# Performance work log

Measured on AMD Instinct MI355X. Metric: run time of the kernel, lower is better.

Reference implementation:

```python
import jax, jax.numpy as jnp
import numpy as np

B = 2048        # graphs
MAX_LEN = 254   # nodes per graph (pad target)
DIM = 64
NF = 78         # num_features_xd
DEG = 8
N = B * MAX_LEN         # 520192 nodes
E = N * DEG             # 4161536 edges
BN_EPS = 1e-5
LN_EPS = 1e-5


def setup_inputs() -> dict:
    key = jax.random.key(0)
    ks = jax.random.split(key, 24)
    x = jax.random.normal(ks[0], (N, NF), jnp.float32)
    # intra-graph random edges: (src, dst) within the same graph
    g = jax.random.randint(ks[1], (E,), 0, B)
    src = g * MAX_LEN + jax.random.randint(ks[2], (E,), 0, MAX_LEN)
    dst = g * MAX_LEN + jax.random.randint(ks[3], (E,), 0, MAX_LEN)
    edge_index = jnp.stack([src, dst]).astype(jnp.int32)
    batch = (jnp.arange(N) // MAX_LEN).astype(jnp.int32)
    batch_len = jnp.full((B,), MAX_LEN, jnp.int32)

    def lin(k, fan_in, shape):
        return jax.random.uniform(k, shape, jnp.float32, -1.0, 1.0) / np.sqrt(fan_in)

    # conv1 MLP: 78->64->64
    w1a = lin(ks[4], NF, (NF, DIM)); b1a = lin(ks[5], NF, (DIM,))
    w1b = lin(ks[6], DIM, (DIM, DIM)); b1b = lin(ks[7], DIM, (DIM,))
    # convs 2-5 stacked: 64->64->64
    Wa = lin(ks[8], DIM, (4, DIM, DIM)); ba = lin(ks[9], DIM, (4, DIM))
    Wb = lin(ks[10], DIM, (4, DIM, DIM)); bb = lin(ks[11], DIM, (4, DIM))
    bn_gamma = jnp.ones((5, DIM), jnp.float32)
    bn_beta = jnp.zeros((5, DIM), jnp.float32)
    fc_w = lin(ks[12], DIM, (DIM, DIM)); fc_b = lin(ks[13], DIM, (DIM,))
    ln_gamma = jnp.ones((DIM,), jnp.float32)
    ln_beta = jnp.zeros((DIM,), jnp.float32)
    return {
        "x": x, "edge_index": edge_index, "batch": batch,
        "batch_len": batch_len, "max_len": MAX_LEN,
        "w1a": w1a, "b1a": b1a, "w1b": w1b, "b1b": b1b,
        "Wa": Wa, "ba": ba, "Wb": Wb, "bb": bb,
        "bn_gamma": bn_gamma, "bn_beta": bn_beta,
        "fc_w": fc_w, "fc_b": fc_b,
        "ln_gamma": ln_gamma, "ln_beta": ln_beta,
    }


def _gin_layer(h, src, dst, n, W1, b1, W2, b2, gamma, beta):
    # GINConv (eps=0): z_i = MLP(x_i + sum_{j->i} x_j), then ReLU, then BatchNorm (batch stats)
    agg = jax.ops.segment_sum(h[src], dst, num_segments=n)
    z = h + agg
    z = jnp.maximum(z @ W1 + b1, 0.0) @ W2 + b2
    z = jnp.maximum(z, 0.0)
    mean = z.mean(axis=0)
    var = jnp.square(z - mean).mean(axis=0)  # biased var, as torch BN training
    return (z - mean) * jax.lax.rsqrt(var + BN_EPS) * gamma + beta


def reference(x, edge_index, batch, batch_len, max_len,
              w1a, b1a, w1b, b1b, Wa, ba, Wb, bb,
              bn_gamma, bn_beta, fc_w, fc_b, ln_gamma, ln_beta):
    n = x.shape[0]
    src, dst = edge_index[0], edge_index[1]
    h = _gin_layer(x, src, dst, n, w1a, b1a, w1b, b1b, bn_gamma[0], bn_beta[0])
    for i in range(4):
        h = _gin_layer(h, src, dst, n, Wa[i], ba[i], Wb[i], bb[i],
                       bn_gamma[i + 1], bn_beta[i + 1])
    # get_nodes_att_f: pad per-graph node features to [B, max_len, dim]
    nb = batch_len.shape[0]
    offsets = jnp.cumsum(batch_len) - batch_len            # start index of each graph
    pos = jnp.arange(n, dtype=jnp.int32) - offsets[batch]  # node position within graph
    x_seq = jnp.zeros((nb, max_len, h.shape[1]), h.dtype).at[batch, pos].set(h)
    # global_add_pool + fc + relu + (dropout eval: identity) + layernorm
    pooled = jax.ops.segment_sum(h, batch, num_segments=nb)
    y = jnp.maximum(pooled @ fc_w + fc_b, 0.0)
    mu = y.mean(axis=-1, keepdims=True)
    var = jnp.square(y - mu).mean(axis=-1, keepdims=True)
    y = (y - mu) * jax.lax.rsqrt(var + LN_EPS) * ln_gamma + ln_beta
    return (x_seq, y)
```

## Files before the change

kernel.cpp:

```cpp
#include <hip/hip_runtime.h>

#define NGRAPH 2048
#define MAXLEN 254
#define NNODE 520192
#define NEDGE 4161536
#define NF 78
#define CAP 32
#define BN_EPS 1e-5f
#define LN_EPS 1e-5f

__global__ __launch_bounds__(256) void k_init(int* __restrict__ deg, float* __restrict__ stats) {
    int i = blockIdx.x * 256 + threadIdx.x;
    deg[i] = 0;
    if (blockIdx.x == 0) {
        for (int j = threadIdx.x; j < 5 * 128; j += 256) stats[j] = 0.f;
    }
}

__global__ __launch_bounds__(256) void k_build(const int* __restrict__ ei,
                                               int* __restrict__ deg,
                                               unsigned char* __restrict__ elist) {
    int e = blockIdx.x * 256 + threadIdx.x;
    int s = ei[e];
    int d = ei[NEDGE + e];
    int g = d / MAXLEN;
    int r = atomicAdd(&deg[d], 1);
    elist[(size_t)d * CAP + r] = (unsigned char)(s - g * MAXLEN);
}

template <int FOLD>
__global__ __launch_bounds__(256) void k_gather(const float* __restrict__ h,
                                                const unsigned char* __restrict__ elist,
                                                const int* __restrict__ deg,
                                                const float* __restrict__ stats,
                                                const float* __restrict__ gamma,
                                                const float* __restrict__ beta,
                                                float* __restrict__ acc) {
    const int CHUNK = (NNODE * 16 / 256) / 8;
    int lb = (int)(blockIdx.x & 7) * CHUNK + (int)(blockIdx.x >> 3);
    size_t t = (size_t)lb * 256 + threadIdx.x;
    int node = (int)(t >> 4);
    int g4 = (int)(t & 15) * 4;
    int dg = deg[node];
    int base = (node / MAXLEN) * MAXLEN;
    const float4 h0 = *(const float4*)(h + ((size_t)node << 6) + g4);
    float a0 = h0.x, a1 = h0.y, a2 = h0.z, a3 = h0.w;
    const unsigned* row = (const unsigned*)(elist + (size_t)node * CAP);
    int ne4 = (dg + 3) >> 2;
    for (int e4 = 0; e4 < ne4; e4++) {
        unsigned pk = row[e4];
#pragma unroll
        for (int j = 0; j < 4; j++) {
            if (4 * e4 + j < dg) {
                int s = base + (int)((pk >> (8 * j)) & 255u);
                float4 v = *(const float4*)(h + ((size_t)s << 6) + g4);
                a0 += v.x; a1 += v.y; a2 += v.z; a3 += v.w;
            }
        }
    }
    if (FOLD) {
        const float invN = 1.0f / NNODE;
        float k = (float)(1 + dg);
        float r[4] = {a0, a1, a2, a3};
#pragma unroll
        for (int j = 0; j < 4; j++) {
            float mean = stats[g4 + j] * invN;
            float var = stats[64 + g4 + j] * invN - mean * mean;
            float sc = gamma[g4 + j] * rsqrtf(var + BN_EPS);
            float bi = beta[g4 + j] - mean * sc;
            r[j] = r[j] * sc + k * bi;
        }
        a0 = r[0]; a1 = r[1]; a2 = r[2]; a3 = r[3];
    }
    *(float4*)(acc + ((size_t)node << 6) + g4) = make_float4(a0, a1, a2, a3);
}

__global__ __launch_bounds__(256) void k_gemm78(const float* __restrict__ x,
                                                const float* __restrict__ W,
                                                float* __restrict__ out) {
    __shared__ float sW[NF * 64];
    for (int i = threadIdx.x; i < NF * 64; i += 256) sW[i] = W[i];
    __syncthreads();
    int node = blockIdx.x * 256 + threadIdx.x;
    const float* xr = x + (size_t)node * NF;
    float a[64];
#pragma unroll
    for (int c = 0; c < 64; c++) a[c] = 0.f;
    for (int k2 = 0; k2 < NF / 2; k2++) {
        float2 xv = ((const float2*)xr)[k2];
        const float* w0 = sW + (2 * k2) * 64;
#pragma unroll
        for (int c = 0; c < 64; c++) a[c] += xv.x * w0[c];
#pragma unroll
        for (int c = 0; c < 64; c++) a[c] += xv.y * w0[64 + c];
    }
    float* orow = out + ((size_t)node << 6);
#pragma unroll
    for (int c = 0; c < 64; c += 4)
        *(float4*)(orow + c) = make_float4(a[c], a[c + 1], a[c + 2], a[c + 3]);
}

__device__ __forceinline__ void second_matmul(const float (&a)[64], const float* __restrict__ sW2,
                                              const float* __restrict__ sb2,
                                              float* __restrict__ orow) {
#pragma unroll
    for (int cb = 0; cb < 64; cb += 16) {
        float o[16];
#pragma unroll
        for (int j = 0; j < 16; j++) o[j] = sb2[cb + j];
#pragma unroll
        for (int k = 0; k < 64; k++) {
            float ak = a[k];
#pragma unroll
            for (int j = 0; j < 16; j++) o[j] += ak * sW2[k * 64 + cb + j];
        }
#pragma unroll
        for (int j = 0; j < 16; j += 4)
            *(float4*)(orow + cb + j) =
                make_float4(fmaxf(o[j], 0.f), fmaxf(o[j + 1], 0.f),
                            fmaxf(o[j + 2], 0.f), fmaxf(o[j + 3], 0.f));
    }
}

__global__ __launch_bounds__(256) void k_mlp_tail(const float* __restrict__ zin,
                                                  const float* __restrict__ b1,
                                                  const float* __restrict__ W2,
                                                  const float* __restrict__ b2,
                                                  float* __restrict__ out) {
    __shared__ float sW2[64 * 64];
    __shared__ float sb1[64], sb2[64];
    for (int i = threadIdx.x; i < 64 * 64; i += 256) sW2[i] = W2[i];
    if (threadIdx.x < 64) { sb1[threadIdx.x] = b1[threadIdx.x]; sb2[threadIdx.x] = b2[threadIdx.x]; }
    __syncthreads();
    int node = blockIdx.x * 256 + threadIdx.x;
    const float* zr = zin + ((size_t)node << 6);
    float a[64];
#pragma unroll
    for (int c = 0; c < 64; c += 4) {
        float4 v = *(const float4*)(zr + c);
        a[c]     = fmaxf(v.x + sb1[c], 0.f);
        a[c + 1] = fmaxf(v.y + sb1[c + 1], 0.f);
        a[c + 2] = fmaxf(v.z + sb1[c + 2], 0.f);
        a[c + 3] = fmaxf(v.w + sb1[c + 3], 0.f);
    }
    second_matmul(a, sW2, sb2, out + ((size_t)node << 6));
}

__global__ __launch_bounds__(256) void k_mlp_dual(const float* __restrict__ zin,
                                                  const float* __restrict__ W1,
                                                  const float* __restrict__ b1,
                                                  const float* __restrict__ W2,
                                                  const float* __restrict__ b2,
                                                  float* __restrict__ out) {
    __shared__ float sW1[64 * 64];
    __shared__ float sW2[64 * 64];
    __shared__ float sb1[64], sb2[64];
    for (int i = threadIdx.x; i < 64 * 64; i += 256) { sW1[i] = W1[i]; sW2[i] = W2[i]; }
    if (threadIdx.x < 64) { sb1[threadIdx.x] = b1[threadIdx.x]; sb2[threadIdx.x] = b2[threadIdx.x]; }
    __syncthreads();
    int node = blockIdx.x * 256 + threadIdx.x;
    const float* zr = zin + ((size_t)node << 6);
    float a[64];
#pragma unroll
    for (int c = 0; c < 64; c++) a[c] = sb1[c];
    for (int k4 = 0; k4 < 16; k4++) {
        float4 xv = ((const float4*)zr)[k4];
        const float* w = sW1 + k4 * 256;
#pragma unroll
        for (int c = 0; c < 64; c++) a[c] += xv.x * w[c];
#pragma unroll
        for (int c = 0; c < 64; c++) a[c] += xv.y * w[64 + c];
#pragma unroll
        for (int c = 0; c < 64; c++) a[c] += xv.z * w[128 + c];
#pragma unroll
        for (int c = 0; c < 64; c++) a[c] += xv.w * w[192 + c];
    }
#pragma unroll
    for (int c = 0; c < 64; c++) a[c] = fmaxf(a[c], 0.f);
    second_matmul(a, sW2, sb2, out + ((size_t)node << 6));
}

__global__ __launch_bounds__(256) void k_bnstats(const float* __restrict__ h,
                                                 float* __restrict__ stats) {
    __shared__ float ss[128];
    if (threadIdx.x < 128) ss[threadIdx.x] = 0.f;
    __syncthreads();
    int tid = blockIdx.x * 256 + threadIdx.x;
    int c4 = (tid & 15) * 4;
    float s0 = 0, s1 = 0, s2 = 0, s3 = 0, q0 = 0, q1 = 0, q2 = 0, q3 = 0;
    const float4* p = (const float4*)h;
    for (size_t i = tid; i < (size_t)NNODE * 16; i += 65536) {
        float4 v = p[i];
        s0 += v.x; q0 += v.x * v.x;
        s1 += v.y; q1 += v.y * v.y;
        s2 += v.z; q2 += v.z * v.z;
        s3 += v.w; q3 += v.w * v.w;
    }
    atomicAdd(&ss[c4], s0);      atomicAdd(&ss[c4 + 1], s1);
    atomicAdd(&ss[c4 + 2], s2);  atomicAdd(&ss[c4 + 3], s3);
    atomicAdd(&ss[64 + c4], q0); atomicAdd(&ss[64 + c4 + 1], q1);
    atomicAdd(&ss[64 + c4 + 2], q2); atomicAdd(&ss[64 + c4 + 3], q3);
    __syncthreads();
    if (threadIdx.x < 128) atomicAdd(&stats[threadIdx.x], ss[threadIdx.x]);
}

__global__ __launch_bounds__(256) void k_bnapply(float* __restrict__ h,
                                                 const float* __restrict__ stats,
                                                 const float* __restrict__ gamma,
                                                 const float* __restrict__ beta) {
    size_t i = (size_t)blockIdx.x * 256 + threadIdx.x;
    int c0 = (int)(i & 15) * 4;
    const float invN = 1.0f / NNODE;
    float4 v = ((const float4*)h)[i];
    float sc[4], bi[4];
#pragma unroll
    for (int j = 0; j < 4; j++) {
        float mean = stats[c0 + j] * invN;
        float var = stats[64 + c0 + j] * invN - mean * mean;
        float s = gamma[c0 + j] * rsqrtf(var + BN_EPS);
        sc[j] = s;
        bi[j] = beta[c0 + j] - mean * s;
    }
    v.x = v.x * sc[0] + bi[0];
    v.y = v.y * sc[1] + bi[1];
    v.z = v.z * sc[2] + bi[2];
    v.w = v.w * sc[3] + bi[3];
    ((float4*)h)[i] = v;
}

__global__ __launch_bounds__(256) void k_final(const float* __restrict__ h,
                                               const float* __restrict__ fcw,
                                               const float* __restrict__ fcb,
                                               const float* __restrict__ lng,
                                               const float* __restrict__ lnb,
                                               float* __restrict__ y) {
    int b = blockIdx.x;
    int q = threadIdx.x >> 6;
    int c = threadIdx.x & 63;
    const float* base = h + (size_t)b * MAXLEN * 64;
    float s = 0.f;
    for (int p = q; p < MAXLEN; p += 4) s += base[p * 64 + c];
    __shared__ float sp[4][64];
    sp[q][c] = s;
    __syncthreads();
    __shared__ float pooled[64];
    if (threadIdx.x < 64) pooled[c] = sp[0][c] + sp[1][c] + sp[2][c] + sp[3][c];
    __syncthreads();
    if (threadIdx.x < 64) {
        float accv = fcb[c];
        for (int k = 0; k < 64; k++) accv += pooled[k] * fcw[k * 64 + c];
        accv = fmaxf(accv, 0.f);
        float t = accv;
        for (int o = 32; o; o >>= 1) t += __shfl_xor(t, o, 64);
        float mu = t * (1.0f / 64.0f);
        float d = accv - mu;
        float t2 = d * d;
        for (int o = 32; o; o >>= 1) t2 += __shfl_xor(t2, o, 64);
        float var = t2 * (1.0f / 64.0f);
        y[(size_t)b * 64 + c] = d * rsqrtf(var + LN_EPS) * lng[c] + lnb[c];
    }
}

extern "C" void kernel_launch(void* const* d_in, const int* in_sizes, int n_in,
                              void* d_out, int out_size, void* d_ws, size_t ws_size,
                              hipStream_t stream) {
    const float* x   = (const float*)d_in[0];
    const int*   ei  = (const int*)d_in[1];
    const float* w1a = (const float*)d_in[5];
    const float* b1a = (const float*)d_in[6];
    const float* w1b = (const float*)d_in[7];
    const float* b1b = (const float*)d_in[8];
    const float* Wa  = (const float*)d_in[9];
    const float* ba  = (const float*)d_in[10];
    const float* Wb  = (const float*)d_in[11];
    const float* bb  = (const float*)d_in[12];
    const float* bng = (const float*)d_in[13];
    const float* bnb = (const float*)d_in[14];
    const float* fcw = (const float*)d_in[15];
    const float* fcb = (const float*)d_in[16];
    const float* lng = (const float*)d_in[17];
    const float* lnb = (const float*)d_in[18];

    float* h   = (float*)d_out;
    float* y   = h + (size_t)NNODE * 64;
    float* acc = (float*)d_ws;
    float* stats = acc + (size_t)NNODE * 64;
    int* deg = (int*)(stats + 5 * 128);
    unsigned char* elist = (unsigned char*)(deg + NNODE);

    const int NB_NODE = NNODE / 256;
    const int NB_VEC  = NNODE * 16 / 256;
    const int NB_EDGE = NEDGE / 256;
    (void)in_sizes; (void)n_in; (void)out_size; (void)ws_size;

    k_init<<<NB_NODE, 256, 0, stream>>>(deg, stats);
    k_build<<<NB_EDGE, 256, 0, stream>>>(ei, deg, elist);

    k_gemm78<<<NB_NODE, 256, 0, stream>>>(x, w1a, h);
    k_gather<0><<<NB_VEC, 256, 0, stream>>>(h, elist, deg, nullptr, nullptr, nullptr, acc);
    k_mlp_tail<<<NB_NODE, 256, 0, stream>>>(acc, b1a, w1b, b1b, h);
    k_bnstats<<<256, 256, 0, stream>>>(h, stats);

    for (int L = 1; L <= 4; L++) {
        k_gather<1><<<NB_VEC, 256, 0, stream>>>(h, elist, deg,
                                                stats + (L - 1) * 128,
                                                bng + (size_t)(L - 1) * 64,
                                                bnb + (size_t)(L - 1) * 64, acc);
        k_mlp_dual<<<NB_NODE, 256, 0, stream>>>(acc, Wa + (size_t)(L - 1) * 4096,
                                                ba + (size_t)(L - 1) * 64,
                                                Wb + (size_t)(L - 1) * 4096,
                                                bb + (size_t)(L - 1) * 64, h);
        k_bnstats<<<256, 256, 0, stream>>>(h, stats + L * 128);
    }

    k_bnapply<<<NB_VEC, 256, 0, stream>>>(h, stats + 4 * 128, bng + 4 * 64, bnb + 4 * 64);
    k_final<<<NGRAPH, 256, 0, stream>>>(h, fcw, fcb, lng, lnb, y);
}
```

Before: 2.321 ms.

## Fuse neighbor gather into per-node MLP kernel and fold final BN into pooling

Replaces the separate gather kernel plus MLP kernel with a single per-layer kernel in which each thread aggregates a full 64-wide node row from its neighbors and then runs both matmuls. Layer outputs ping-pong between two buffers. The final BatchNorm apply is moved into the pooling kernel. This removes the intermediate accumulator write and re-read and several launches. The cost is much higher register pressure (two 64-float arrays), and gathers become uncoalesced, since each thread reads whole 256-byte rows instead of 16 lanes sharing a row.

New measurement: 3.717 ms. 1.6x slower.

```diff
diff --git a/kernel.cpp b/kernel.cpp
--- a/kernel.cpp
+++ b/kernel.cpp
@@ -28,53 +28,6 @@
     elist[(size_t)d * CAP + r] = (unsigned char)(s - g * MAXLEN);
 }
 
-template <int FOLD>
-__global__ __launch_bounds__(256) void k_gather(const float* __restrict__ h,
-                                                const unsigned char* __restrict__ elist,
-                                                const int* __restrict__ deg,
-                                                const float* __restrict__ stats,
-                                                const float* __restrict__ gamma,
-                                                const float* __restrict__ beta,
-                                                float* __restrict__ acc) {
-    const int CHUNK = (NNODE * 16 / 256) / 8;
-    int lb = (int)(blockIdx.x & 7) * CHUNK + (int)(blockIdx.x >> 3);
-    size_t t = (size_t)lb * 256 + threadIdx.x;
-    int node = (int)(t >> 4);
-    int g4 = (int)(t & 15) * 4;
-    int dg = deg[node];
-    int base = (node / MAXLEN) * MAXLEN;
-    const float4 h0 = *(const float4*)(h + ((size_t)node << 6) + g4);
-    float a0 = h0.x, a1 = h0.y, a2 = h0.z, a3 = h0.w;
-    const unsigned* row = (const unsigned*)(elist + (size_t)node * CAP);
-    int ne4 = (dg + 3) >> 2;
-    for (int e4 = 0; e4 < ne4; e4++) {
-        unsigned pk = row[e4];
-#pragma unroll
-        for (int j = 0; j < 4; j++) {
-            if (4 * e4 + j < dg) {
-                int s = base + (int)((pk >> (8 * j)) & 255u);
-                float4 v = *(const float4*)(h + ((size_t)s << 6) + g4);
-                a0 += v.x; a1 += v.y; a2 += v.z; a3 += v.w;
-            }
-        }
-    }
-    if (FOLD) {
-        const float invN = 1.0f / NNODE;
-        float k = (float)(1 + dg);
-        float r[4] = {a0, a1, a2, a3};
-#pragma unroll
-        for (int j = 0; j < 4; j++) {
-            float mean = stats[g4 + j] * invN;
-            float var = stats[64 + g4 + j] * invN - mean * mean;
-            float sc = gamma[g4 + j] * rsqrtf(var + BN_EPS);
-            float bi = beta[g4 + j] - mean * sc;
-            r[j] = r[j] * sc + k * bi;
-        }
-        a0 = r[0]; a1 = r[1]; a2 = r[2]; a3 = r[3];
-    }
-    *(float4*)(acc + ((size_t)node << 6) + g4) = make_float4(a0, a1, a2, a3);
-}
-
 __global__ __launch_bounds__(256) void k_gemm78(const float* __restrict__ x,
                                                 const float* __restrict__ W,
                                                 float* __restrict__ out) {
@@ -122,62 +75,98 @@
     }
 }
 
-__global__ __launch_bounds__(256) void k_mlp_tail(const float* __restrict__ zin,
-                                                  const float* __restrict__ b1,
-                                                  const float* __restrict__ W2,
-                                                  const float* __restrict__ b2,
-                                                  float* __restrict__ out) {
+template <int FIRST, int FOLD>
+__global__ __launch_bounds__(256) void k_layer(const float* __restrict__ hin,
+                                               const unsigned char* __restrict__ elist,
+                                               const int* __restrict__ deg,
+                                               const float* __restrict__ stats,
+                                               const float* __restrict__ gamma,
+                                               const float* __restrict__ beta,
+                                               const float* __restrict__ W1,
+                                               const float* __restrict__ b1,
+                                               const float* __restrict__ W2,
+                                               const float* __restrict__ b2,
+                                               float* __restrict__ hout) {
+    __shared__ float sW1[FIRST ? 1 : 64 * 64];
     __shared__ float sW2[64 * 64];
     __shared__ float sb1[64], sb2[64];
+    __shared__ float ssc[64], sbi[64];
+    if (!FIRST)
+        for (int i = threadIdx.x; i < 64 * 64; i += 256) sW1[i] = W1[i];
     for (int i = threadIdx.x; i < 64 * 64; i += 256) sW2[i] = W2[i];
-    if (threadIdx.x < 64) { sb1[threadIdx.x] = b1[threadIdx.x]; sb2[threadIdx.x] = b2[threadIdx.x]; }
-    __syncthreads();
-    int node = blockIdx.x * 256 + threadIdx.x;
-    const float* zr = zin + ((size_t)node << 6);
+    if (threadIdx.x < 64) {
+        sb1[threadIdx.x] = b1[threadIdx.x];
+        sb2[threadIdx.x] = b2[threadIdx.x];
+        if (FOLD) {
+            const float invN = 1.0f / NNODE;
+            int c = threadIdx.x;
+            float mean = stats[c] * invN;
+            float var = stats[64 + c] * invN - mean * mean;
+            float sc = gamma[c] * rsqrtf(var + BN_EPS);
+            ssc[c] = sc;
+            sbi[c] = beta[c] - mean * sc;
+        }
+    }
+    __syncthreads();
+
+    int lb = (int)(blockIdx.x & 7) * 254 + (int)(blockIdx.x >> 3);
+    int node = lb * 256 + threadIdx.x;
+    int dg = deg[node];
+    int base = (node / MAXLEN) * MAXLEN;
+
+    float g[64];
+    const float* hr = hin + ((size_t)node << 6);
+#pragma unroll
+    for (int c4 = 0; c4 < 16; c4++) {
+        float4 v = ((const float4*)hr)[c4];
+        g[4 * c4] = v.x; g[4 * c4 + 1] = v.y; g[4 * c4 + 2] = v.z; g[4 * c4 + 3] = v.w;
+    }
+    const unsigned* row = (const unsigned*)(elist + (size_t)node * CAP);
+    int ne4 = (dg + 3) >> 2;
+    for (int e4 = 0; e4 < ne4; e4++) {
+        unsigned pk = row[e4];
+#pragma unroll
+        for (int j = 0; j < 4; j++) {
+            if (4 * e4 + j < dg) {
+                const float* sr = hin + ((size_t)(base + (int)((pk >> (8 * j)) & 255u)) << 6);
+#pragma unroll
+                for (int c4 = 0; c4 < 16; c4++) {
+                    float4 v = ((const float4*)sr)[c4];
+                    g[4 * c4] += v.x; g[4 * c4 + 1] += v.y;
+                    g[4 * c4 + 2] += v.z; g[4 * c4 + 3] += v.w;
+                }
+            }
+        }
+    }
+    if (FOLD) {
+        float kk = (float)(1 + dg);
+#pragma unroll
+        for (int c = 0; c < 64; c++) g[c] = g[c] * ssc[c] + kk * sbi[c];
+    }
+
     float a[64];
-#pragma unroll
-    for (int c = 0; c < 64; c += 4) {
-        float4 v = *(const float4*)(zr + c);
-        a[c]     = fmaxf(v.x + sb1[c], 0.f);
-        a[c + 1] = fmaxf(v.y + sb1[c + 1], 0.f);
-        a[c + 2] = fmaxf(v.z + sb1[c + 2], 0.f);
-        a[c + 3] = fmaxf(v.w + sb1[c + 3], 0.f);
-    }
-    second_matmul(a, sW2, sb2, out + ((size_t)node << 6));
-}
-
-__global__ __launch_bounds__(256) void k_mlp_dual(const float* __restrict__ zin,
-                                                  const float* __restrict__ W1,
-                                                  const float* __restrict__ b1,
-                                                  const float* __restrict__ W2,
-                                                  const float* __restrict__ b2,
-                                                  float* __restrict__ out) {
-    __shared__ float sW1[64 * 64];
-    __shared__ float sW2[64 * 64];
-    __shared__ float sb1[64], sb2[64];
-    for (int i = threadIdx.x; i < 64 * 64; i += 256) { sW1[i] = W1[i]; sW2[i] = W2[i]; }
-    if (threadIdx.x < 64) { sb1[threadIdx.x] = b1[threadIdx.x]; sb2[threadIdx.x] = b2[threadIdx.x]; }
-    __syncthreads();
-    int node = blockIdx.x * 256 + threadIdx.x;
-    const float* zr = zin + ((size_t)node << 6);
-    float a[64];
-#pragma unroll
-    for (int c = 0; c < 64; c++) a[c] = sb1[c];
-    for (int k4 = 0; k4 < 16; k4++) {
-        float4 xv = ((const float4*)zr)[k4];
-        const float* w = sW1 + k4 * 256;
-#pragma unroll
-        for (int c = 0; c < 64; c++) a[c] += xv.x * w[c];
-#pragma unroll
-        for (int c = 0; c < 64; c++) a[c] += xv.y * w[64 + c];
-#pragma unroll
-        for (int c = 0; c < 64; c++) a[c] += xv.z * w[128 + c];
-#pragma unroll
-        for (int c = 0; c < 64; c++) a[c] += xv.w * w[192 + c];
-    }
-#pragma unroll
-    for (int c = 0; c < 64; c++) a[c] = fmaxf(a[c], 0.f);
-    second_matmul(a, sW2, sb2, out + ((size_t)node << 6));
+    if (FIRST) {
+#pragma unroll
+        for (int c = 0; c < 64; c++) a[c] = fmaxf(g[c] + sb1[c], 0.f);
+    } else {
+#pragma unroll
+        for (int c = 0; c < 64; c++) a[c] = sb1[c];
+        for (int k4 = 0; k4 < 16; k4++) {
+            const float* w = sW1 + k4 * 256;
+            float g0 = g[4 * k4], g1 = g[4 * k4 + 1], g2 = g[4 * k4 + 2], g3 = g[4 * k4 + 3];
+#pragma unroll
+            for (int c = 0; c < 64; c++) a[c] += g0 * w[c];
+#pragma unroll
+            for (int c = 0; c < 64; c++) a[c] += g1 * w[64 + c];
+#pragma unroll
+            for (int c = 0; c < 64; c++) a[c] += g2 * w[128 + c];
+#pragma unroll
+            for (int c = 0; c < 64; c++) a[c] += g3 * w[192 + c];
+        }
+#pragma unroll
+        for (int c = 0; c < 64; c++) a[c] = fmaxf(a[c], 0.f);
+    }
+    second_matmul(a, sW2, sb2, hout + ((size_t)node << 6));
 }
 
 __global__ __launch_bounds__(256) void k_bnstats(const float* __restrict__ h,
@@ -204,31 +193,10 @@
     if (threadIdx.x < 128) atomicAdd(&stats[threadIdx.x], ss[threadIdx.x]);
 }
 
-__global__ __launch_bounds__(256) void k_bnapply(float* __restrict__ h,
-                                                 const float* __restrict__ stats,
-                                                 const float* __restrict__ gamma,
-                                                 const float* __restrict__ beta) {
-    size_t i = (size_t)blockIdx.x * 256 + threadIdx.x;
-    int c0 = (int)(i & 15) * 4;
-    const float invN = 1.0f / NNODE;
-    float4 v = ((const float4*)h)[i];
-    float sc[4], bi[4];
-#pragma unroll
-    for (int j = 0; j < 4; j++) {
-        float mean = stats[c0 + j] * invN;
-        float var = stats[64 + c0 + j] * invN - mean * mean;
-        float s = gamma[c0 + j] * rsqrtf(var + BN_EPS);
-        sc[j] = s;
-        bi[j] = beta[c0 + j] - mean * s;
-    }
-    v.x = v.x * sc[0] + bi[0];
-    v.y = v.y * sc[1] + bi[1];
-    v.z = v.z * sc[2] + bi[2];
-    v.w = v.w * sc[3] + bi[3];
-    ((float4*)h)[i] = v;
-}
-
-__global__ __launch_bounds__(256) void k_final(const float* __restrict__ h,
+__global__ __launch_bounds__(256) void k_final(float* __restrict__ h,
+                                               const float* __restrict__ stats,
+                                               const float* __restrict__ gamma,
+                                               const float* __restrict__ beta,
                                                const float* __restrict__ fcw,
                                                const float* __restrict__ fcb,
                                                const float* __restrict__ lng,
@@ -237,9 +205,24 @@
     int b = blockIdx.x;
     int q = threadIdx.x >> 6;
     int c = threadIdx.x & 63;
-    const float* base = h + (size_t)b * MAXLEN * 64;
+    __shared__ float ssc[64], sbi[64];
+    if (threadIdx.x < 64) {
+        const float invN = 1.0f / NNODE;
+        float mean = stats[c] * invN;
+        float var = stats[64 + c] * invN - mean * mean;
+        float sc = gamma[c] * rsqrtf(var + BN_EPS);
+        ssc[c] = sc;
+        sbi[c] = beta[c] - mean * sc;
+    }
+    __syncthreads();
+    float* base = h + (size_t)b * MAXLEN * 64;
+    float sc = ssc[c], bi = sbi[c];
     float s = 0.f;
-    for (int p = q; p < MAXLEN; p += 4) s += base[p * 64 + c];
+    for (int p = q; p < MAXLEN; p += 4) {
+        float v = base[p * 64 + c] * sc + bi;
+        base[p * 64 + c] = v;
+        s += v;
+    }
     __shared__ float sp[4][64];
     sp[q][c] = s;
     __syncthreads();
@@ -289,30 +272,31 @@
     unsigned char* elist = (unsigned char*)(deg + NNODE);
 
     const int NB_NODE = NNODE / 256;
-    const int NB_VEC  = NNODE * 16 / 256;
     const int NB_EDGE = NEDGE / 256;
     (void)in_sizes; (void)n_in; (void)out_size; (void)ws_size;
 
     k_init<<<NB_NODE, 256, 0, stream>>>(deg, stats);
     k_build<<<NB_EDGE, 256, 0, stream>>>(ei, deg, elist);
 
-    k_gemm78<<<NB_NODE, 256, 0, stream>>>(x, w1a, h);
-    k_gather<0><<<NB_VEC, 256, 0, stream>>>(h, elist, deg, nullptr, nullptr, nullptr, acc);
-    k_mlp_tail<<<NB_NODE, 256, 0, stream>>>(acc, b1a, w1b, b1b, h);
+    k_gemm78<<<NB_NODE, 256, 0, stream>>>(x, w1a, acc);
+    k_layer<1, 0><<<NB_NODE, 256, 0, stream>>>(acc, elist, deg, nullptr, nullptr, nullptr,
+                                               nullptr, b1a, w1b, b1b, h);
     k_bnstats<<<256, 256, 0, stream>>>(h, stats);
 
     for (int L = 1; L <= 4; L++) {
-        k_gather<1><<<NB_VEC, 256, 0, stream>>>(h, elist, deg,
-                                                stats + (L - 1) * 128,
-                                                bng + (size_t)(L - 1) * 64,
-                                                bnb + (size_t)(L - 1) * 64, acc);
-        k_mlp_dual<<<NB_NODE, 256, 0, stream>>>(acc, Wa + (size_t)(L - 1) * 4096,
-                                                ba + (size_t)(L - 1) * 64,
-                                                Wb + (size_t)(L - 1) * 4096,
-                                                bb + (size_t)(L - 1) * 64, h);
-        k_bnstats<<<256, 256, 0, stream>>>(h, stats + L * 128);
-    }
-
-    k_bnapply<<<NB_VEC, 256, 0, stream>>>(h, stats + 4 * 128, bng + 4 * 64, bnb + 4 * 64);
-    k_final<<<NGRAPH, 256, 0, stream>>>(h, fcw, fcb, lng, lnb, y);
-}
+        const float* in = (L & 1) ? h : acc;
+        float* out      = (L & 1) ? acc : h;
+        k_layer<0, 1><<<NB_NODE, 256, 0, stream>>>(in, elist, deg,
+                                                   stats + (L - 1) * 128,
+                                                   bng + (size_t)(L - 1) * 64,
+                                                   bnb + (size_t)(L - 1) * 64,
+                                                   Wa + (size_t)(L - 1) * 4096,
+                                                   ba + (size_t)(L - 1) * 64,
+                                                   Wb + (size_t)(L - 1) * 4096,
+                                                   bb + (size_t)(L - 1) * 64, out);
+        k_bnstats<<<256, 256, 0, stream>>>(out, stats + L * 128);
+    }
+
+    k_final<<<NGRAPH, 256, 0, stream>>>(h, stats + 4 * 128, bng + 4 * 64, bnb + 4 * 64,
+                                        fcw, fcb, lng, lnb, y);
+}
```
